# Optimization experiments

Hardware: AMD Instinct MI355X
Metric: run time of the kernel (lower is better)

The kernel has to match this reference:

```python
import jax, jax.numpy as jnp
import numpy as np
import math

N, S, T, E, H = 2, 2048, 2048, 1024, 16
HD = E // H  # head_dim = 64


def setup_inputs() -> dict:
    key = jax.random.key(0)
    ks = jax.random.split(key, 11)
    scale = 1.0 / math.sqrt(E)
    inp = {
        "query": jax.random.normal(ks[0], (N, S, E), jnp.float32),
        "key": jax.random.normal(ks[1], (N, T, E), jnp.float32),
        "value": jax.random.normal(ks[2], (N, T, E), jnp.float32),
        "Wq": jax.random.normal(ks[3], (E, E), jnp.float32) * scale,
        "bq": jnp.zeros((E,), jnp.float32),
        "Wk": jax.random.normal(ks[4], (E, E), jnp.float32) * scale,
        "bk": jnp.zeros((E,), jnp.float32),
        "Wv": jax.random.normal(ks[5], (E, E), jnp.float32) * scale,
        "bv": jnp.zeros((E,), jnp.float32),
        "Wo": jax.random.normal(ks[6], (E, E), jnp.float32) * scale,
        "bo": jnp.zeros((E,), jnp.float32),
    }
    return inp


def reference(query, key, value, Wq, bq, Wk, bk, Wv, bv, Wo, bo):
    # QKV projections, then split heads: [N, S, E] -> [N, H, S, HD]
    q = (query @ Wq + bq).reshape(N, S, H, HD).transpose(0, 2, 1, 3)
    k = (key @ Wk + bk).reshape(N, T, H, HD).transpose(0, 2, 1, 3)
    v = (value @ Wv + bv).reshape(N, T, H, HD).transpose(0, 2, 1, 3)
    # scaled dot-product attention scores [N, H, S, T]
    scores = jnp.einsum('nhse,nhte->nhst', q, k) / math.sqrt(HD)
    attn = jax.nn.softmax(scores, axis=-1)
    # dropout is identity in eval mode
    out = jnp.einsum('nhst,nhte->nhse', attn, v)  # [N, H, S, HD]
    out = out.transpose(0, 2, 1, 3).reshape(N, S, E)
    return out @ Wo + bo
```

## Files before the change

### kernel.cpp

```cpp
#include <hip/hip_runtime.h>
#include <hip/hip_bf16.h>

typedef __bf16 bf16x8 __attribute__((ext_vector_type(8)));
typedef __bf16 bf16x4 __attribute__((ext_vector_type(4)));
typedef float  f32x4  __attribute__((ext_vector_type(4)));
typedef float  f32x16 __attribute__((ext_vector_type(16)));
typedef unsigned int u32x4 __attribute__((ext_vector_type(4)));

#define MFMA16(a, b, c) __builtin_amdgcn_mfma_f32_16x16x32_bf16((a), (b), (c), 0, 0, 0)
#define MFMA32(a, b, c) __builtin_amdgcn_mfma_f32_32x32x16_bf16((a), (b), (c), 0, 0, 0)

constexpr int SEQ = 2048, EMB = 1024, NHEAD = 16, HD = 64;
constexpr float SSCALE = 0.18033688f;

__device__ __forceinline__ void glds16(const void* g, void* l) {
    __builtin_amdgcn_global_load_lds(
        (const __attribute__((address_space(1))) void*)g,
        (__attribute__((address_space(3))) void*)l, 16, 0, 0);
}

__global__ __launch_bounds__(256)
void prep(const float* __restrict__ W0, const float* __restrict__ W1,
          const float* __restrict__ W2, const float* __restrict__ W3,
          __bf16* __restrict__ T0, __bf16* __restrict__ T1,
          __bf16* __restrict__ T2, __bf16* __restrict__ T3,
          const float* __restrict__ X0, const float* __restrict__ X1,
          const float* __restrict__ X2, __bf16* __restrict__ Y0,
          __bf16* __restrict__ Y1, __bf16* __restrict__ Y2)
{
    __shared__ float tile[32][33];
    const int z = blockIdx.z;
    if (z < 4) {
        const float* W = (z==0) ? W0 : (z==1) ? W1 : (z==2) ? W2 : W3;
        __bf16*      T = (z==0) ? T0 : (z==1) ? T1 : (z==2) ? T2 : T3;
        const float s = (z == 0) ? SSCALE : 1.0f;
        const int kb = blockIdx.x * 32, nb = blockIdx.y * 32;
        const int c = threadIdx.x & 31, r0 = threadIdx.x >> 5;
#pragma unroll
        for (int i = 0; i < 4; ++i)
            tile[r0 + 8*i][c] = W[(size_t)(kb + r0 + 8*i)*1024 + nb + c];
        __syncthreads();
#pragma unroll
        for (int i = 0; i < 4; ++i)
            T[(size_t)(nb + r0 + 8*i)*1024 + kb + c] = (__bf16)(tile[c][r0 + 8*i] * s);
    } else {
        const float* X = (z==4) ? X0 : (z==5) ? X1 : X2;
        __bf16*      Y = (z==4) ? Y0 : (z==5) ? Y1 : Y2;
        const size_t base =
            ((size_t)(blockIdx.y * 32 + blockIdx.x) * 256 + threadIdx.x) * 16;
#pragma unroll
        for (int j = 0; j < 2; ++j) {
            const float4* s4 = (const float4*)(X + base + j*8);
            float4 f0 = s4[0], f1 = s4[1];
            bf16x8 v;
            v[0]=(__bf16)f0.x; v[1]=(__bf16)f0.y; v[2]=(__bf16)f0.z; v[3]=(__bf16)f0.w;
            v[4]=(__bf16)f1.x; v[5]=(__bf16)f1.y; v[6]=(__bf16)f1.z; v[7]=(__bf16)f1.w;
            *(bf16x8*)(Y + base + j*8) = v;
        }
    }
}

struct GArg { const __bf16* A; const __bf16* Bt; const float* bias; void* C;
              int mode; int kbase; int kcount; float bscale; };
struct GArgs3 { GArg a[3]; };

__global__ __launch_bounds__(256)
void gemmk(GArgs3 args)
{
    const int lin = blockIdx.x + (blockIdx.y << 5) + (blockIdx.z << 8);
    const int nid = (lin & 7) * 96 + (lin >> 3);
    const int gz = nid >> 8, rem = nid & 255;
    const int bm = rem >> 3, bn = rem & 7;
    const GArg g = args.a[gz];
    __shared__ __attribute__((aligned(16))) __bf16 sm[4*128*64];
    const int tid = threadIdx.x, lane = tid & 63, wave = tid >> 6;
    const int wm = wave >> 1, wn = wave & 1;
    const int quad = lane >> 4, l16 = lane & 15;

    const __bf16* ap[4];
    const __bf16* bp[4];
#pragma unroll
    for (int j = 0; j < 4; ++j) {
        const int ci = j*256 + tid;
        const int row = ci >> 3, cg = ((ci & 7) ^ (row & 7)) * 8;
        ap[j] = g.A  + (size_t)(bm*128 + row)*1024 + g.kbase + cg;
        bp[j] = g.Bt + (size_t)(bn*128 + row)*1024 + g.kbase + cg;
    }

    auto stage = [&](int b) {
        __bf16* Ad = sm + b * 16384;
        __bf16* Bd = Ad + 8192;
#pragma unroll
        for (int j = 0; j < 4; ++j) {
            glds16(ap[j], &Ad[(j*256 + wave*64)*8]);
            glds16(bp[j], &Bd[(j*256 + wave*64)*8]);
            ap[j] += 64; bp[j] += 64;
        }
    };

    f32x4 acc[4][4] = {};

    stage(0);
    int cur = 0;
    for (int kt = 0; kt < g.kcount; ++kt) {
        __syncthreads();
        if (kt < g.kcount - 1) stage(cur ^ 1);
        const __bf16* As = sm + cur * 16384;
        const __bf16* Bs = As + 8192;
#pragma unroll
        for (int ks = 0; ks < 2; ++ks) {
            const int kc = ks*4 + quad;
            bf16x8 af[4], bfr[4];
#pragma unroll
            for (int mt = 0; mt < 4; ++mt) {
                const int ar = wm*64 + mt*16 + l16;
                af[mt] = *(const bf16x8*)&As[ar*64 + (kc ^ (ar & 7))*8];
            }
#pragma unroll
            for (int nt = 0; nt < 4; ++nt) {
                const int br = wn*64 + nt*16 + l16;
                bfr[nt] = *(const bf16x8*)&Bs[br*64 + (kc ^ (br & 7))*8];
            }
#pragma unroll
            for (int mt = 0; mt < 4; ++mt)
#pragma unroll
                for (int nt = 0; nt < 4; ++nt)
                    acc[mt][nt] = MFMA16(af[mt], bfr[nt], acc[mt][nt]);
        }
        cur ^= 1;
    }

    if (g.mode == 0) {
        __syncthreads();
        __bf16* Cs = sm;
#pragma unroll
        for (int nt = 0; nt < 4; ++nt) {
            const int n = wn*64 + nt*16 + l16;
            const float bvs = g.bias[bn*128 + n] * g.bscale;
#pragma unroll
            for (int mt = 0; mt < 4; ++mt) {
                const int mb = wm*64 + mt*16 + quad*4;
                f32x4 v = acc[mt][nt];
#pragma unroll
                for (int r = 0; r < 4; ++r) {
                    const int m = mb + r;
                    Cs[m*128 + (((n >> 3) ^ (m & 7)) * 8) + (n & 7)] =
                        (__bf16)(v[r] + bvs);
                }
            }
        }
        __syncthreads();
        __bf16* C = (__bf16*)g.C;
        const int p8 = tid & 7;
#pragma unroll
        for (int ps = 0; ps < 8; ++ps) {
            const int run = ps * 32 + (tid >> 3);
            const int m = run >> 1, hh = run & 1;
            const int gm = bm*128 + m;
            const int nb = gm >> 11, s = gm & 2047;
            const int h = bn*2 + hh;
            bf16x8 val = *(const bf16x8*)&Cs[m*128 + (((hh*8 + p8) ^ (m & 7)) * 8)];
            *(bf16x8*)&C[(size_t)(nb*NHEAD + h)*(SEQ*HD) + (size_t)s*HD + p8*8] = val;
        }
    } else {
#pragma unroll
        for (int nt = 0; nt < 4; ++nt) {
            const int n = bn*128 + wn*64 + nt*16 + l16;
            const float bvs = (g.bias ? g.bias[n] : 0.f) * g.bscale;
#pragma unroll
            for (int mt = 0; mt < 4; ++mt) {
                const int mbase = bm*128 + wm*64 + mt*16 + quad*4;
                f32x4 v = acc[mt][nt];
                __bf16* C = (__bf16*)g.C;
                const int h = n >> 6, d = n & 63;
                const int nb = mbase >> 11, s = mbase & 2047;
                const int tg = (s >> 2) & 7;
                const int pg = (tg & 4) | ((tg & 1) << 1) | ((tg & 2) >> 1);
                const int sp = (s & ~31) | (pg << 2);
                bf16x4 o;
#pragma unroll
                for (int r = 0; r < 4; ++r) o[r] = (__bf16)(v[r] + bvs);
                *(bf16x4*)&C[(size_t)(nb*NHEAD + h)*(SEQ*HD) + (size_t)d*SEQ + sp] = o;
            }
        }
    }
}

__global__ __launch_bounds__(256)
void gemmo(const __bf16* __restrict__ A, const __bf16* __restrict__ Bt,
           const float* __restrict__ bias, float* __restrict__ C)
{
    const int lin = blockIdx.x + (blockIdx.y << 5);
    const int nid = (lin & 7) * 32 + (lin >> 3);
    const int bm = nid >> 3, bn = nid & 7;
    __shared__ __attribute__((aligned(16))) __bf16 sm[4*128*64];
    const int tid = threadIdx.x, lane = tid & 63, wave = tid >> 6;
    const int wm = wave >> 1, wn = wave & 1;
    const int quad = lane >> 4, l16 = lane & 15;

    const __bf16* ap[4];
    const __bf16* bp[4];
#pragma unroll
    for (int j = 0; j < 4; ++j) {
        const int ci = j*256 + tid;
        const int row = ci >> 3, cg = ((ci & 7) ^ (row & 7)) * 8;
        ap[j] = A  + (size_t)(bm*128 + row)*1024 + cg;
        bp[j] = Bt + (size_t)(bn*128 + row)*1024 + cg;
    }

    auto stage = [&](int b) {
        __bf16* Ad = sm + b * 16384;
        __bf16* Bd = Ad + 8192;
#pragma unroll
        for (int j = 0; j < 4; ++j) {
            glds16(ap[j], &Ad[(j*256 + wave*64)*8]);
            glds16(bp[j], &Bd[(j*256 + wave*64)*8]);
            ap[j] += 64; bp[j] += 64;
        }
    };

    f32x4 acc[4][4] = {};

    stage(0);
    int cur = 0;
    for (int kt = 0; kt < 16; ++kt) {
        __syncthreads();
        if (kt < 15) stage(cur ^ 1);
        const __bf16* As = sm + cur * 16384;
        const __bf16* Bs = As + 8192;
#pragma unroll
        for (int ks = 0; ks < 2; ++ks) {
            const int kc = ks*4 + quad;
            bf16x8 af[4], bfr[4];
#pragma unroll
            for (int mt = 0; mt < 4; ++mt) {
                const int ar = wm*64 + mt*16 + l16;
                af[mt] = *(const bf16x8*)&As[ar*64 + (kc ^ (ar & 7))*8];
            }
#pragma unroll
            for (int nt = 0; nt < 4; ++nt) {
                const int br = wn*64 + nt*16 + l16;
                bfr[nt] = *(const bf16x8*)&Bs[br*64 + (kc ^ (br & 7))*8];
            }
#pragma unroll
            for (int mt = 0; mt < 4; ++mt)
#pragma unroll
                for (int nt = 0; nt < 4; ++nt)
                    acc[mt][nt] = MFMA16(af[mt], bfr[nt], acc[mt][nt]);
        }
        cur ^= 1;
    }
#pragma unroll
    for (int nt = 0; nt < 4; ++nt) {
        const int n = bn*128 + wn*64 + nt*16 + l16;
        const float bv = bias[n];
#pragma unroll
        for (int mt = 0; mt < 4; ++mt) {
            const int mbase = bm*128 + wm*64 + mt*16 + quad*4;
            f32x4 v = acc[mt][nt];
#pragma unroll
            for (int r = 0; r < 4; ++r)
                C[(size_t)(mbase + r)*1024 + n] = v[r] + bv;
        }
    }
}

__global__ __launch_bounds__(512, 2)
void attn32(const __bf16* __restrict__ qg, const __bf16* __restrict__ kg,
            const __bf16* __restrict__ vg, __bf16* __restrict__ Og)
{
    __shared__ __attribute__((aligned(16))) char smem[64*1024];
    float* Xch = (float*)smem;

    const int tid = threadIdx.x, lane = tid & 63, wave = tid >> 6;
    const int w4 = wave & 3, grp = wave >> 2;
    const int l32 = lane & 31, half = lane >> 5;
    const int nh = blockIdx.y;
    const int q0 = blockIdx.x * 128;
    const __bf16* qb = qg + (size_t)nh * (SEQ*HD);
    const __bf16* kb = kg + (size_t)nh * (SEQ*HD);
    const __bf16* vb = vg + (size_t)nh * (SEQ*HD);

    bf16x8 qf[4];
#pragma unroll
    for (int ks = 0; ks < 4; ++ks)
        qf[ks] = *(const bf16x8*)(qb + (size_t)(q0 + w4*32 + l32)*HD + ks*16 + half*8);

    f32x16 oacc[2] = {};
    float psum = 0.0f;

    const int cK0 = tid, rK0 = cK0 >> 3;
    const int cK1 = 512 + tid, rK1 = cK1 >> 3;
    const __bf16* kp0 = kb + (size_t)rK0*HD + ((cK0 & 7) ^ (rK0 & 7)) * 8;
    const __bf16* kp1 = kb + (size_t)rK1*HD + ((cK1 & 7) ^ (rK1 & 7)) * 8;
    const int cV0 = tid, rV0 = cV0 >> 4, pV0 = cV0 & 15;
    const int cV1 = 512 + tid, rV1 = cV1 >> 4, pV1 = cV1 & 15;
    const __bf16* vp0 = vb + (size_t)rV0*SEQ + (((pV0 & ~7) | ((pV0 & 7) ^ (rV0 & 7))) * 8);
    const __bf16* vp1 = vb + (size_t)rV1*SEQ + (((pV1 & ~7) | ((pV1 & 7) ^ (rV1 & 7))) * 8);

    auto stage = [&](int b) {
        char* Kd = smem + b * 16384;
        char* Vd = smem + 32768 + b * 16384;
        glds16(kp0, Kd + wave*1024);
        glds16(kp1, Kd + 8192 + wave*1024);
        glds16(vp0, Vd + wave*1024);
        glds16(vp1, Vd + 8192 + wave*1024);
        kp0 += 128*HD; kp1 += 128*HD;
        vp0 += 128;    vp1 += 128;
    };

    stage(0);
    int cur = 0;
    for (int it = 0; it < 16; ++it) {
        __syncthreads();
        if (it < 15) stage(cur ^ 1);

        const __bf16* Ks = (const __bf16*)(smem + cur * 16384);
        const __bf16* Vs = (const __bf16*)(smem + 32768 + cur * 16384);

        f32x16 sc[2] = {};
        __builtin_amdgcn_s_setprio(1);
#pragma unroll
        for (int ks = 0; ks < 4; ++ks) {
            const int c = ks*2 + half;
#pragma unroll
            for (int nt = 0; nt < 2; ++nt) {
                const int kr = grp*64 + nt*32 + l32;
                bf16x8 kf = *(const bf16x8*)&Ks[kr*64 + ((c ^ (kr & 7))*8)];
                sc[nt] = MFMA32(kf, qf[ks], sc[nt]);
            }
        }
        __builtin_amdgcn_s_setprio(0);

#pragma unroll
        for (int nt = 0; nt < 2; ++nt)
#pragma unroll
            for (int sub = 0; sub < 2; ++sub) {
                const float e0 = __builtin_amdgcn_exp2f(sc[nt][sub*8 + 0]);
                const float e1 = __builtin_amdgcn_exp2f(sc[nt][sub*8 + 1]);
                const float e2 = __builtin_amdgcn_exp2f(sc[nt][sub*8 + 2]);
                const float e3 = __builtin_amdgcn_exp2f(sc[nt][sub*8 + 3]);
                const float e4 = __builtin_amdgcn_exp2f(sc[nt][sub*8 + 4]);
                const float e5 = __builtin_amdgcn_exp2f(sc[nt][sub*8 + 5]);
                const float e6 = __builtin_amdgcn_exp2f(sc[nt][sub*8 + 6]);
                const float e7 = __builtin_amdgcn_exp2f(sc[nt][sub*8 + 7]);
                psum += ((e0 + e1) + (e2 + e3)) + ((e4 + e5) + (e6 + e7));
                u32x4 pk;
                asm("v_cvt_pk_bf16_f32 %0, %1, %2" : "=v"(pk.x) : "v"(e0), "v"(e1));
                asm("v_cvt_pk_bf16_f32 %0, %1, %2" : "=v"(pk.y) : "v"(e2), "v"(e3));
                asm("v_cvt_pk_bf16_f32 %0, %1, %2" : "=v"(pk.z) : "v"(e4), "v"(e5));
                asm("v_cvt_pk_bf16_f32 %0, %1, %2" : "=v"(pk.w) : "v"(e6), "v"(e7));
                const bf16x8 pf = __builtin_bit_cast(bf16x8, pk);
                const int c2 = grp*8 + (nt*2 + sub)*2 + half;
                __builtin_amdgcn_s_setprio(1);
#pragma unroll
                for (int dt = 0; dt < 2; ++dt) {
                    const int vr = dt*32 + l32;
                    const int pos = (c2 & ~7) | ((c2 & 7) ^ (vr & 7));
                    bf16x8 vf = *(const bf16x8*)&Vs[vr*128 + pos*8];
                    oacc[dt] = MFMA32(pf, vf, oacc[dt]);
                }
                __builtin_amdgcn_s_setprio(0);
            }
        cur ^= 1;
    }

    __syncthreads();
    if (grp == 1) {
        float* dst = &Xch[((w4*64) + lane) * 33];
#pragma unroll
        for (int i = 0; i < 16; ++i) {
            dst[i]      = oacc[0][i];
            dst[16 + i] = oacc[1][i];
        }
        dst[32] = psum;
    }
    __syncthreads();
    if (grp == 0) {
        const float* src = &Xch[((w4*64) + lane) * 33];
#pragma unroll
        for (int i = 0; i < 16; ++i) {
            oacc[0][i] += src[i];
            oacc[1][i] += src[16 + i];
        }
        psum += src[32];
        psum += __shfl(psum, lane ^ 32);
        float* dl = (float*)(smem + 60*1024);
        if (half == 0) dl[w4*32 + l32] = psum;
        const int nb = nh >> 4, h = nh & 15;
#pragma unroll
        for (int reg = 0; reg < 16; ++reg) {
            const int row = (reg & 3) + 8*(reg >> 2) + 4*half;
            const int srow = q0 + w4*32 + row;
            const float inv = 1.0f / dl[w4*32 + row];
#pragma unroll
            for (int dt = 0; dt < 2; ++dt)
                Og[(size_t)(nb*SEQ + srow)*EMB + h*HD + dt*32 + l32] =
                    (__bf16)(oacc[dt][reg] * inv);
        }
    }
}

extern "C" void kernel_launch(void* const* d_in, const int* in_sizes, int n_in,
                              void* d_out, int out_size, void* d_ws, size_t ws_size,
                              hipStream_t stream)
{
    const float* query = (const float*)d_in[0];
    const float* key_  = (const float*)d_in[1];
    const float* value = (const float*)d_in[2];
    const float* Wq = (const float*)d_in[3];
    const float* bq = (const float*)d_in[4];
    const float* Wk = (const float*)d_in[5];
    const float* bk = (const float*)d_in[6];
    const float* Wv = (const float*)d_in[7];
    const float* bv = (const float*)d_in[8];
    const float* Wo = (const float*)d_in[9];
    const float* bo = (const float*)d_in[10];
    float* out = (float*)d_out;

    constexpr size_t SZW = 1024u*1024u;
    constexpr size_t SZX = 4096u*1024u;
    __bf16* ws  = (__bf16*)d_ws;
    __bf16* WqT = ws;
    __bf16* WkT = WqT + SZW;
    __bf16* WvT = WkT + SZW;
    __bf16* WoT = WvT + SZW;
    __bf16* xv  = WoT + SZW;
    __bf16* qh  = xv + SZX;
    __bf16* kh  = qh + SZX;
    __bf16* vTh = kh + SZX;
    __bf16* xq  = (__bf16*)d_out;
    __bf16* xk  = xq + SZX;
    __bf16* Oh  = xv;

    prep<<<dim3(32, 32, 7), 256, 0, stream>>>(Wq, Wk, Wv, Wo, WqT, WkT, WvT, WoT,
                                              query, key_, value, xq, xk, xv);
    GArgs3 a;
    a.a[0] = { xq, WqT, bq, qh,  0, 0, 16, SSCALE };
    a.a[1] = { xk, WkT, bk, kh,  0, 0, 16, 1.0f };
    a.a[2] = { xv, WvT, bv, vTh, 1, 0, 16, 1.0f };
    gemmk<<<dim3(32, 8, 3), 256, 0, stream>>>(a);
    attn32<<<dim3(16, 32), 512, 0, stream>>>(qh, kh, vTh, Oh);
    gemmo<<<dim3(32, 8), 256, 0, stream>>>(Oh, WoT, bo, out);
}
```

Baseline: 209.8 us.

## Remap attention waves so each K fragment feeds two query tiles

Reassigns the eight waves in the attention kernel so each wave owns 64 query rows (two 32-row Q tiles) and a 32-key slice of each K/V block, instead of 32 query rows and a 64-key slice. Each K fragment and V fragment read from LDS now feeds two MFMAs, which halves LDS fragment reads per MFMA. In exchange, each wave holds twice the Q and output accumulator registers. The cross-wave reduction also grows to four partials per query tile, done in two LDS exchange rounds with extra barriers and explicit lgkm waits.

```diff
diff --git a/kernel.cpp b/kernel.cpp
--- a/kernel.cpp
+++ b/kernel.cpp
@@ -9,6 +9,8 @@
 
 #define MFMA16(a, b, c) __builtin_amdgcn_mfma_f32_16x16x32_bf16((a), (b), (c), 0, 0, 0)
 #define MFMA32(a, b, c) __builtin_amdgcn_mfma_f32_32x32x16_bf16((a), (b), (c), 0, 0, 0)
+#define LGKM_FENCE() do { asm volatile("s_waitcnt lgkmcnt(0)" ::: "memory"); \
+                          __builtin_amdgcn_sched_barrier(0); } while (0)
 
 constexpr int SEQ = 2048, EMB = 1024, NHEAD = 16, HD = 64;
 constexpr float SSCALE = 0.18033688f;
@@ -266,28 +268,31 @@
 }
 
 __global__ __launch_bounds__(512, 2)
-void attn32(const __bf16* __restrict__ qg, const __bf16* __restrict__ kg,
+void attn32(const __bf16* __restrict__ qg_, const __bf16* __restrict__ kg,
             const __bf16* __restrict__ vg, __bf16* __restrict__ Og)
 {
     __shared__ __attribute__((aligned(16))) char smem[64*1024];
     float* Xch = (float*)smem;
 
     const int tid = threadIdx.x, lane = tid & 63, wave = tid >> 6;
-    const int w4 = wave & 3, grp = wave >> 2;
+    const int tq = wave & 3, qh = wave >> 2;
     const int l32 = lane & 31, half = lane >> 5;
     const int nh = blockIdx.y;
     const int q0 = blockIdx.x * 128;
-    const __bf16* qb = qg + (size_t)nh * (SEQ*HD);
+    const __bf16* qb = qg_ + (size_t)nh * (SEQ*HD);
     const __bf16* kb = kg + (size_t)nh * (SEQ*HD);
     const __bf16* vb = vg + (size_t)nh * (SEQ*HD);
 
-    bf16x8 qf[4];
-#pragma unroll
-    for (int ks = 0; ks < 4; ++ks)
-        qf[ks] = *(const bf16x8*)(qb + (size_t)(q0 + w4*32 + l32)*HD + ks*16 + half*8);
-
-    f32x16 oacc[2] = {};
-    float psum = 0.0f;
+    bf16x8 qf[2][4];
+#pragma unroll
+    for (int qg = 0; qg < 2; ++qg)
+#pragma unroll
+        for (int ks = 0; ks < 4; ++ks)
+            qf[qg][ks] = *(const bf16x8*)(qb +
+                (size_t)(q0 + qh*64 + qg*32 + l32)*HD + ks*16 + half*8);
+
+    f32x16 oacc[2][2] = {};
+    float psum0 = 0.0f, psum1 = 0.0f;
 
     const int cK0 = tid, rK0 = cK0 >> 3;
     const int cK1 = 512 + tid, rK1 = cK1 >> 3;
@@ -318,86 +323,123 @@
         const __bf16* Ks = (const __bf16*)(smem + cur * 16384);
         const __bf16* Vs = (const __bf16*)(smem + 32768 + cur * 16384);
 
-        f32x16 sc[2] = {};
+        f32x16 sc0 = {}, sc1 = {};
+        const int kr = tq*32 + l32;
         __builtin_amdgcn_s_setprio(1);
 #pragma unroll
         for (int ks = 0; ks < 4; ++ks) {
             const int c = ks*2 + half;
-#pragma unroll
-            for (int nt = 0; nt < 2; ++nt) {
-                const int kr = grp*64 + nt*32 + l32;
-                bf16x8 kf = *(const bf16x8*)&Ks[kr*64 + ((c ^ (kr & 7))*8)];
-                sc[nt] = MFMA32(kf, qf[ks], sc[nt]);
-            }
+            bf16x8 kf = *(const bf16x8*)&Ks[kr*64 + ((c ^ (kr & 7))*8)];
+            sc0 = MFMA32(kf, qf[0][ks], sc0);
+            sc1 = MFMA32(kf, qf[1][ks], sc1);
         }
         __builtin_amdgcn_s_setprio(0);
 
 #pragma unroll
-        for (int nt = 0; nt < 2; ++nt)
-#pragma unroll
-            for (int sub = 0; sub < 2; ++sub) {
-                const float e0 = __builtin_amdgcn_exp2f(sc[nt][sub*8 + 0]);
-                const float e1 = __builtin_amdgcn_exp2f(sc[nt][sub*8 + 1]);
-                const float e2 = __builtin_amdgcn_exp2f(sc[nt][sub*8 + 2]);
-                const float e3 = __builtin_amdgcn_exp2f(sc[nt][sub*8 + 3]);
-                const float e4 = __builtin_amdgcn_exp2f(sc[nt][sub*8 + 4]);
-                const float e5 = __builtin_amdgcn_exp2f(sc[nt][sub*8 + 5]);
-                const float e6 = __builtin_amdgcn_exp2f(sc[nt][sub*8 + 6]);
-                const float e7 = __builtin_amdgcn_exp2f(sc[nt][sub*8 + 7]);
-                psum += ((e0 + e1) + (e2 + e3)) + ((e4 + e5) + (e6 + e7));
-                u32x4 pk;
-                asm("v_cvt_pk_bf16_f32 %0, %1, %2" : "=v"(pk.x) : "v"(e0), "v"(e1));
-                asm("v_cvt_pk_bf16_f32 %0, %1, %2" : "=v"(pk.y) : "v"(e2), "v"(e3));
-                asm("v_cvt_pk_bf16_f32 %0, %1, %2" : "=v"(pk.z) : "v"(e4), "v"(e5));
-                asm("v_cvt_pk_bf16_f32 %0, %1, %2" : "=v"(pk.w) : "v"(e6), "v"(e7));
-                const bf16x8 pf = __builtin_bit_cast(bf16x8, pk);
-                const int c2 = grp*8 + (nt*2 + sub)*2 + half;
-                __builtin_amdgcn_s_setprio(1);
-#pragma unroll
-                for (int dt = 0; dt < 2; ++dt) {
-                    const int vr = dt*32 + l32;
-                    const int pos = (c2 & ~7) | ((c2 & 7) ^ (vr & 7));
-                    bf16x8 vf = *(const bf16x8*)&Vs[vr*128 + pos*8];
-                    oacc[dt] = MFMA32(pf, vf, oacc[dt]);
-                }
-                __builtin_amdgcn_s_setprio(0);
-            }
+        for (int sub = 0; sub < 2; ++sub) {
+            float ea[8], eb[8];
+#pragma unroll
+            for (int j = 0; j < 8; ++j) {
+                ea[j] = __builtin_amdgcn_exp2f(sc0[sub*8 + j]);
+                eb[j] = __builtin_amdgcn_exp2f(sc1[sub*8 + j]);
+            }
+            psum0 += ((ea[0]+ea[1]) + (ea[2]+ea[3])) + ((ea[4]+ea[5]) + (ea[6]+ea[7]));
+            psum1 += ((eb[0]+eb[1]) + (eb[2]+eb[3])) + ((eb[4]+eb[5]) + (eb[6]+eb[7]));
+            u32x4 pka, pkb;
+            asm("v_cvt_pk_bf16_f32 %0, %1, %2" : "=v"(pka.x) : "v"(ea[0]), "v"(ea[1]));
+            asm("v_cvt_pk_bf16_f32 %0, %1, %2" : "=v"(pka.y) : "v"(ea[2]), "v"(ea[3]));
+            asm("v_cvt_pk_bf16_f32 %0, %1, %2" : "=v"(pka.z) : "v"(ea[4]), "v"(ea[5]));
+            asm("v_cvt_pk_bf16_f32 %0, %1, %2" : "=v"(pka.w) : "v"(ea[6]), "v"(ea[7]));
+            asm("v_cvt_pk_bf16_f32 %0, %1, %2" : "=v"(pkb.x) : "v"(eb[0]), "v"(eb[1]));
+            asm("v_cvt_pk_bf16_f32 %0, %1, %2" : "=v"(pkb.y) : "v"(eb[2]), "v"(eb[3]));
+            asm("v_cvt_pk_bf16_f32 %0, %1, %2" : "=v"(pkb.z) : "v"(eb[4]), "v"(eb[5]));
+            asm("v_cvt_pk_bf16_f32 %0, %1, %2" : "=v"(pkb.w) : "v"(eb[6]), "v"(eb[7]));
+            const bf16x8 pf0 = __builtin_bit_cast(bf16x8, pka);
+            const bf16x8 pf1 = __builtin_bit_cast(bf16x8, pkb);
+            const int c2 = tq*4 + sub*2 + half;
+            __builtin_amdgcn_s_setprio(1);
+#pragma unroll
+            for (int dt = 0; dt < 2; ++dt) {
+                const int vr = dt*32 + l32;
+                const int pos = (c2 & ~7) | ((c2 & 7) ^ (vr & 7));
+                bf16x8 vf = *(const bf16x8*)&Vs[vr*128 + pos*8];
+                oacc[0][dt] = MFMA32(pf0, vf, oacc[0][dt]);
+                oacc[1][dt] = MFMA32(pf1, vf, oacc[1][dt]);
+            }
+            __builtin_amdgcn_s_setprio(0);
+        }
         cur ^= 1;
     }
 
     __syncthreads();
-    if (grp == 1) {
-        float* dst = &Xch[((w4*64) + lane) * 33];
+    if (tq != 0) {
+        float* dst = &Xch[(((qh*3) + (tq-1))*64 + lane) * 33];
 #pragma unroll
         for (int i = 0; i < 16; ++i) {
-            dst[i]      = oacc[0][i];
-            dst[16 + i] = oacc[1][i];
-        }
-        dst[32] = psum;
+            dst[i]      = oacc[0][0][i];
+            dst[16 + i] = oacc[0][1][i];
+        }
+        dst[32] = psum0;
+        LGKM_FENCE();
     }
     __syncthreads();
-    if (grp == 0) {
-        const float* src = &Xch[((w4*64) + lane) * 33];
+    if (tq == 0) {
+#pragma unroll
+        for (int s = 0; s < 3; ++s) {
+            const float* src = &Xch[(((qh*3) + s)*64 + lane) * 33];
+#pragma unroll
+            for (int i = 0; i < 16; ++i) {
+                oacc[0][0][i] += src[i];
+                oacc[0][1][i] += src[16 + i];
+            }
+            psum0 += src[32];
+        }
+        LGKM_FENCE();
+    }
+    __syncthreads();
+    if (tq != 0) {
+        float* dst = &Xch[(((qh*3) + (tq-1))*64 + lane) * 33];
 #pragma unroll
         for (int i = 0; i < 16; ++i) {
-            oacc[0][i] += src[i];
-            oacc[1][i] += src[16 + i];
-        }
-        psum += src[32];
-        psum += __shfl(psum, lane ^ 32);
+            dst[i]      = oacc[1][0][i];
+            dst[16 + i] = oacc[1][1][i];
+        }
+        dst[32] = psum1;
+        LGKM_FENCE();
+    }
+    __syncthreads();
+    if (tq == 0) {
+#pragma unroll
+        for (int s = 0; s < 3; ++s) {
+            const float* src = &Xch[(((qh*3) + s)*64 + lane) * 33];
+#pragma unroll
+            for (int i = 0; i < 16; ++i) {
+                oacc[1][0][i] += src[i];
+                oacc[1][1][i] += src[16 + i];
+            }
+            psum1 += src[32];
+        }
+        psum0 += __shfl(psum0, lane ^ 32);
+        psum1 += __shfl(psum1, lane ^ 32);
         float* dl = (float*)(smem + 60*1024);
-        if (half == 0) dl[w4*32 + l32] = psum;
+        if (half == 0) {
+            dl[qh*64 + l32]      = psum0;
+            dl[qh*64 + 32 + l32] = psum1;
+        }
+        LGKM_FENCE();
         const int nb = nh >> 4, h = nh & 15;
 #pragma unroll
-        for (int reg = 0; reg < 16; ++reg) {
-            const int row = (reg & 3) + 8*(reg >> 2) + 4*half;
-            const int srow = q0 + w4*32 + row;
-            const float inv = 1.0f / dl[w4*32 + row];
-#pragma unroll
-            for (int dt = 0; dt < 2; ++dt)
-                Og[(size_t)(nb*SEQ + srow)*EMB + h*HD + dt*32 + l32] =
-                    (__bf16)(oacc[dt][reg] * inv);
-        }
+        for (int qg = 0; qg < 2; ++qg)
+#pragma unroll
+            for (int reg = 0; reg < 16; ++reg) {
+                const int row = (reg & 3) + 8*(reg >> 2) + 4*half;
+                const int srow = q0 + qh*64 + qg*32 + row;
+                const float inv = 1.0f / dl[qh*64 + qg*32 + row];
+#pragma unroll
+                for (int dt = 0; dt < 2; ++dt)
+                    Og[(size_t)(nb*SEQ + srow)*EMB + h*HD + dt*32 + l32] =
+                        (__bf16)(oacc[qg][dt][reg] * inv);
+            }
     }
 }
 
```

Result: slower. 217.4 us (+3.6%).
